# Kernel tuning notes

Measured on AMD Instinct MI355X. Metric: run time of the kernel, lower is better.

Reference implementation:

```python
import jax, jax.numpy as jnp
import numpy as np

NEG_SLOPE = 0.3

def capped_lrelu(x):
    # clamp(LeakyReLU_0.3(x), max=1)
    return jnp.minimum(jnp.where(x >= 0, x, NEG_SLOPE * x), 1.0)

def setup_inputs() -> dict:
    key = jax.random.key(0)
    ks = jax.random.split(key, 8)
    B, T, V, H, O = 64, 512, 512, 256, 512
    s = 1.0 / np.sqrt(H)
    return {
        "sentence": jax.random.normal(ks[0], (B, T, V), dtype=jnp.float32),
        "prev_state": jnp.zeros((1, B, H), dtype=jnp.float32),
        "W_ih": jax.random.normal(ks[1], (H, V), dtype=jnp.float32) * s,
        "b_ih": jax.random.normal(ks[2], (H,), dtype=jnp.float32) * s,
        "W_hh": jax.random.normal(ks[3], (H, H), dtype=jnp.float32) * s,
        "b_hh": jax.random.normal(ks[4], (H,), dtype=jnp.float32) * s,
        "W_out": jax.random.normal(ks[5], (O, H), dtype=jnp.float32) * s,
        "b_out": jax.random.normal(ks[6], (O,), dtype=jnp.float32) * s,
    }

def reference(sentence, prev_state, W_ih, b_ih, W_hh, b_hh, W_out, b_out):
    # nn.RNN(nonlinearity='relu'), batch_first, n_layers=1:
    #   h_t = relu(x_t @ W_ih^T + b_ih + h_{t-1} @ W_hh^T + b_hh)
    # Precompute input projections for all timesteps, scan the recurrence.
    x_proj = jnp.einsum('btv,hv->bth', sentence, W_ih) + b_ih  # [B,T,H]
    x_proj_t = jnp.swapaxes(x_proj, 0, 1)                      # [T,B,H]
    h0 = prev_state[0]                                         # [B,H]

    def step(h, xt):
        h_new = jax.nn.relu(xt + h @ W_hh.T + b_hh)
        return h_new, h_new

    h_last, out_seq = jax.lax.scan(step, h0, x_proj_t)         # [T,B,H]
    out_seq = jnp.swapaxes(out_seq, 0, 1)                      # [B,T,H]

    hidden_activ = capped_lrelu(out_seq)
    tags = jax.nn.sigmoid(jnp.einsum('bth,oh->bto', hidden_activ, W_out) + b_out)
    h_n = h_last[None]                                         # [1,B,H]
    return tags, h_n
```

## Files before the change

### kernel.cpp

```cpp
#include <hip/hip_runtime.h>
#include <hip/hip_bf16.h>


typedef __attribute__((ext_vector_type(8))) _Float16 half8;
typedef __attribute__((ext_vector_type(4))) _Float16 half4;
typedef __attribute__((ext_vector_type(4))) float   floatx4;

__device__ __forceinline__ void lds_barrier() {
    asm volatile("s_waitcnt lgkmcnt(0)\n\ts_barrier" ::: "memory");
}

__global__ void conv_weights(const float* __restrict__ wih, const float* __restrict__ wout,
                             _Float16* __restrict__ out) {
    int idx = blockIdx.x * blockDim.x + threadIdx.x;
    const float* src = (idx < 32768) ? wih : wout;
    int j = idx & 32767;
    float4 v = ((const float4*)src)[j];
    half4 h = { (_Float16)v.x, (_Float16)v.y, (_Float16)v.z, (_Float16)v.w };
    ((half4*)out)[idx] = h;
}

__device__ __forceinline__ void stage_weights_swz(const _Float16* __restrict__ src,
                                                  int rowStrideHalves,
                                                  _Float16* lds) {
    int wave = threadIdx.x >> 6;
    int lane = threadIdx.x & 63;
#pragma unroll
    for (int j = 0; j < 16; j++) {
        int Lb = j * 8192 + wave * 1024 + lane * 16;
        int n  = Lb >> 9;
        int c  = Lb & 511;
        int cs = c ^ ((n & 7) << 4);
        const _Float16* g = src + (size_t)n * rowStrideHalves + (cs >> 1);
        _Float16* l = lds + (j * 8192 + wave * 1024) / 2;
        __builtin_amdgcn_global_load_lds((const __attribute__((address_space(1))) void*)g,
                                         (__attribute__((address_space(3))) void*)l,
                                         16, 0, 0);
    }
    asm volatile("s_waitcnt vmcnt(0)" ::: "memory");
    __syncthreads();
}

__global__ __launch_bounds__(512, 2) void gemm1_xproj(const float* __restrict__ A,
                                                      const _Float16* __restrict__ Bw,
                                                      const float* __restrict__ b_ih,
                                                      const float* __restrict__ b_hh,
                                                      float* __restrict__ C) {
    const int K = 512, N = 256;
    __shared__ _Float16 ldsB[65536];
    int wave = threadIdx.x >> 6;
    int lane = threadIdx.x & 63;
    int row  = lane & 15;
    int quad = lane >> 4;
    int m0 = blockIdx.x * 128 + wave * 16;

    floatx4 acc[16];
#pragma unroll
    for (int i = 0; i < 16; i++) acc[i] = (floatx4){0.f, 0.f, 0.f, 0.f};

    const float* pa = A + (size_t)(m0 + row) * K + quad * 8;
    const char* lb = (const char*)ldsB;

    for (int h = 0; h < 2; h++) {
        if (h) __syncthreads();
        stage_weights_swz(Bw + h * 256, 512, ldsB);

        for (int kk = 0; kk < 256; kk += 32) {
            float4 a0 = *(const float4*)(pa + h * 256 + kk);
            float4 a1 = *(const float4*)(pa + h * 256 + kk + 4);
            half8 a = { (_Float16)a0.x, (_Float16)a0.y, (_Float16)a0.z, (_Float16)a0.w,
                        (_Float16)a1.x, (_Float16)a1.y, (_Float16)a1.z, (_Float16)a1.w };
#pragma unroll
            for (int nt = 0; nt < 16; nt++) {
                int n = nt * 16 + row;
                int byte = n * 512 + ((quad * 16 + kk * 2) ^ ((n & 7) << 4));
                half8 b = *(const half8*)(lb + byte);
                acc[nt] = __builtin_amdgcn_mfma_f32_16x16x32_f16(a, b, acc[nt], 0, 0, 0);
            }
        }
    }
#pragma unroll
    for (int nt = 0; nt < 16; nt++) {
        int n = nt * 16 + row;
        float bn = b_ih[n] + b_hh[n];
#pragma unroll
        for (int r = 0; r < 4; r++) {
            int m = m0 + quad * 4 + r;
            C[(size_t)m * N + n] = acc[nt][r] + bn;
        }
    }
}

__global__ __launch_bounds__(512, 2) void rnn_recur(const float* __restrict__ xp,
                                                    const float* __restrict__ h0,
                                                    const float* __restrict__ W_hh,
                                                    _Float16* __restrict__ hid,
                                                    float* __restrict__ h_n) {
    const int Hh = 256, T = 512, LD = 264;
    int b0   = blockIdx.x * 16;
    int wave = threadIdx.x >> 6;
    int lane = threadIdx.x & 63;
    int c    = lane & 15;
    int q    = lane >> 4;

    half8 wf[2][8];
#pragma unroll
    for (int nt = 0; nt < 2; nt++) {
        int n = (wave * 2 + nt) * 16 + c;
        const float* wr = W_hh + (size_t)n * Hh + q * 8;
#pragma unroll
        for (int kt = 0; kt < 8; kt++) {
            float4 x0 = *(const float4*)(wr + kt * 32);
            float4 x1 = *(const float4*)(wr + kt * 32 + 4);
            wf[nt][kt] = (half8){ (_Float16)x0.x, (_Float16)x0.y, (_Float16)x0.z, (_Float16)x0.w,
                                  (_Float16)x1.x, (_Float16)x1.y, (_Float16)x1.z, (_Float16)x1.w };
        }
    }

    __shared__ _Float16 hb[2][16][264];
    for (int idx = threadIdx.x; idx < 16 * 256; idx += 512) {
        int m = idx >> 8, k = idx & 255;
        hb[0][m][k] = (_Float16)h0[(size_t)(b0 + m) * Hh + k];
    }
    __syncthreads();

    const float* xpb = xp + (size_t)(b0 + c) * T * Hh;
    _Float16* hidb = hid + (size_t)(b0 + c) * T * Hh;

    int noff[2];
#pragma unroll
    for (int nt = 0; nt < 2; nt++) noff[nt] = (wave * 2 + nt) * 16 + q * 4;

    float4 xq0[2], xq1[2];
#pragma unroll
    for (int nt = 0; nt < 2; nt++) {
        xq0[nt] = *(const float4*)(xpb + (size_t)0 * Hh + noff[nt]);
        xq1[nt] = *(const float4*)(xpb + (size_t)1 * Hh + noff[nt]);
    }
    const float* pf0 = xpb + 2 * Hh;
    const float* pf1 = xpb + 3 * Hh;
    _Float16* hp = hidb;

    auto do_step = [&](int parity, float4 (&xq)[2], const float*& pf,
                       bool prefetch, bool last) {
        const _Float16* hr = &hb[parity][0][0];
        floatx4 aA0 = { xq[0].x, xq[0].y, xq[0].z, xq[0].w };
        floatx4 aA1 = { xq[1].x, xq[1].y, xq[1].z, xq[1].w };
        floatx4 aB0 = {0.f,0.f,0.f,0.f}, aB1 = {0.f,0.f,0.f,0.f};
#pragma unroll
        for (int kt = 0; kt < 4; kt++) {
            half8 hfA = *(const half8*)(hr + c * LD + kt * 32 + q * 8);
            half8 hfB = *(const half8*)(hr + c * LD + (kt + 4) * 32 + q * 8);
            aA0 = __builtin_amdgcn_mfma_f32_16x16x32_f16(wf[0][kt],     hfA, aA0, 0, 0, 0);
            aB0 = __builtin_amdgcn_mfma_f32_16x16x32_f16(wf[0][kt + 4], hfB, aB0, 0, 0, 0);
            aA1 = __builtin_amdgcn_mfma_f32_16x16x32_f16(wf[1][kt],     hfA, aA1, 0, 0, 0);
            aB1 = __builtin_amdgcn_mfma_f32_16x16x32_f16(wf[1][kt + 4], hfB, aB1, 0, 0, 0);
        }
        floatx4 acc[2];
        acc[0] = aA0 + aB0;
        acc[1] = aA1 + aB1;

        _Float16* hw = &hb[parity ^ 1][0][0];
#pragma unroll
        for (int nt = 0; nt < 2; nt++) {
            float v0 = fmaxf(acc[nt][0], 0.f);
            float v1 = fmaxf(acc[nt][1], 0.f);
            float v2 = fmaxf(acc[nt][2], 0.f);
            float v3 = fmaxf(acc[nt][3], 0.f);
            half4 hv = { (_Float16)v0, (_Float16)v1, (_Float16)v2, (_Float16)v3 };
            *(half4*)(hw + c * LD + noff[nt]) = hv;
            *(half4*)(hp + noff[nt]) = hv;
            if (last) {
                float4 hn = { v0, v1, v2, v3 };
                *(float4*)(h_n + (size_t)(b0 + c) * Hh + noff[nt]) = hn;
            }
        }
        hp += Hh;
        if (prefetch) {
#pragma unroll
            for (int nt = 0; nt < 2; nt++)
                xq[nt] = *(const float4*)(pf + noff[nt]);
            pf += 2 * Hh;
        }
        lds_barrier();
    };

    for (int t = 0; t < T - 2; t += 2) {
        do_step(0, xq0, pf0, true, false);
        do_step(1, xq1, pf1, true, false);
    }
    do_step(0, xq0, pf0, false, false);
    do_step(1, xq1, pf1, false, true);
}

__global__ __launch_bounds__(512, 2) void gemm3_tags(const _Float16* __restrict__ A,
                                                     const _Float16* __restrict__ Bw,
                                                     const float* __restrict__ bias,
                                                     float* __restrict__ C) {
    const int K = 256, N = 512;
    __shared__ _Float16 ldsB[65536];
    int wave = threadIdx.x >> 6;
    int lane = threadIdx.x & 63;
    int row  = lane & 15;
    int quad = lane >> 4;
    int m0 = blockIdx.x * 128 + wave * 16;
    int nb = blockIdx.y;

    stage_weights_swz(Bw + (size_t)nb * 256 * K, K, ldsB);

    floatx4 acc[16];
#pragma unroll
    for (int i = 0; i < 16; i++) acc[i] = (floatx4){0.f, 0.f, 0.f, 0.f};

    const _Float16* pa = A + (size_t)(m0 + row) * K + quad * 8;
    const char* lb = (const char*)ldsB;
    const _Float16 one = (_Float16)1.0f;

    for (int kk = 0; kk < 256; kk += 32) {
        half8 a = *(const half8*)(pa + kk);
#pragma unroll
        for (int j = 0; j < 8; j++) a[j] = (a[j] < one) ? a[j] : one;
#pragma unroll
        for (int nt = 0; nt < 16; nt++) {
            int n = nt * 16 + row;
            int byte = n * 512 + ((quad * 16 + kk * 2) ^ ((n & 7) << 4));
            half8 b = *(const half8*)(lb + byte);
            acc[nt] = __builtin_amdgcn_mfma_f32_16x16x32_f16(a, b, acc[nt], 0, 0, 0);
        }
    }
#pragma unroll
    for (int nt = 0; nt < 16; nt++) {
        int n = nb * 256 + nt * 16 + row;
        float bn = bias[n];
#pragma unroll
        for (int r = 0; r < 4; r++) {
            int m = m0 + quad * 4 + r;
            float v = acc[nt][r] + bn;
            C[(size_t)m * N + n] = 1.f / (1.f + __expf(-v));
        }
    }
}

extern "C" void kernel_launch(void* const* d_in, const int* in_sizes, int n_in,
                              void* d_out, int out_size, void* d_ws, size_t ws_size,
                              hipStream_t stream) {
    const float* sentence   = (const float*)d_in[0];
    const float* prev_state = (const float*)d_in[1];
    const float* W_ih       = (const float*)d_in[2];
    const float* b_ih       = (const float*)d_in[3];
    const float* W_hh       = (const float*)d_in[4];
    const float* b_hh       = (const float*)d_in[5];
    const float* W_out      = (const float*)d_in[6];
    const float* b_out      = (const float*)d_in[7];

    const size_t WIH_N   = 256u * 512u;
    const size_t WOUT_N  = 512u * 256u;
    const size_t XPROJ_N = 32768u * 256u;
    const size_t HID_N   = 64u * 512u * 256u;

    char* w = (char*)d_ws;
    _Float16* wih_f  = (_Float16*)w;  w += WIH_N * sizeof(_Float16);
    _Float16* wout_f = (_Float16*)w;  w += WOUT_N * sizeof(_Float16);
    float*    xproj  = (float*)w;     w += XPROJ_N * sizeof(float);
    _Float16* hid_f  = (_Float16*)w;  w += HID_N * sizeof(_Float16);

    float* tags = (float*)d_out;
    float* h_n  = (float*)d_out + 16777216;

    conv_weights<<<256, 256, 0, stream>>>(W_ih, W_out, wih_f);

    gemm1_xproj<<<256, 512, 0, stream>>>(sentence, wih_f, b_ih, b_hh, xproj);

    rnn_recur<<<4, 512, 0, stream>>>(xproj, prev_state, W_hh, hid_f, h_n);

    gemm3_tags<<<dim3(256, 2), 512, 0, stream>>>(hid_f, wout_f, b_out, tags);
}
```

Before: 542.6 us.

## Shrink GEMM tiles to 256 threads and move xproj add after recurrence MFMAs

Both GEMMs move from 512-thread blocks with 128KB LDS weight tiles to 256-thread blocks with 64KB tiles. gemm1 now stages K in four 128-wide phases, and gemm3 splits N into four 128-column blocks, so the grids grow to give more blocks and better occupancy on the CUs. In the recurrence, the MFMA accumulators start at zero and the x-projection is added just before the ReLU, which takes the prefetched xproj load off the MFMA dependency chain. The cost is more weight restaging and more barriers per block.

```diff
diff --git a/kernel.cpp b/kernel.cpp
--- a/kernel.cpp
+++ b/kernel.cpp
@@ -20,19 +20,38 @@
     ((half4*)out)[idx] = h;
 }
 
-__device__ __forceinline__ void stage_weights_swz(const _Float16* __restrict__ src,
-                                                  int rowStrideHalves,
-                                                  _Float16* lds) {
+__device__ __forceinline__ void stage_w_256x128(const _Float16* __restrict__ src,
+                                                int rowStrideHalves, _Float16* lds) {
     int wave = threadIdx.x >> 6;
     int lane = threadIdx.x & 63;
 #pragma unroll
     for (int j = 0; j < 16; j++) {
-        int Lb = j * 8192 + wave * 1024 + lane * 16;
+        int Lb = j * 4096 + wave * 1024 + lane * 16;
+        int n  = Lb >> 8;
+        int c  = Lb & 255;
+        int cs = c ^ ((n & 7) << 4);
+        const _Float16* g = src + (size_t)n * rowStrideHalves + (cs >> 1);
+        _Float16* l = lds + (j * 4096 + wave * 1024) / 2;
+        __builtin_amdgcn_global_load_lds((const __attribute__((address_space(1))) void*)g,
+                                         (__attribute__((address_space(3))) void*)l,
+                                         16, 0, 0);
+    }
+    asm volatile("s_waitcnt vmcnt(0)" ::: "memory");
+    __syncthreads();
+}
+
+__device__ __forceinline__ void stage_w_128x256(const _Float16* __restrict__ src,
+                                                int rowStrideHalves, _Float16* lds) {
+    int wave = threadIdx.x >> 6;
+    int lane = threadIdx.x & 63;
+#pragma unroll
+    for (int j = 0; j < 16; j++) {
+        int Lb = j * 4096 + wave * 1024 + lane * 16;
         int n  = Lb >> 9;
         int c  = Lb & 511;
         int cs = c ^ ((n & 7) << 4);
         const _Float16* g = src + (size_t)n * rowStrideHalves + (cs >> 1);
-        _Float16* l = lds + (j * 8192 + wave * 1024) / 2;
+        _Float16* l = lds + (j * 4096 + wave * 1024) / 2;
         __builtin_amdgcn_global_load_lds((const __attribute__((address_space(1))) void*)g,
                                          (__attribute__((address_space(3))) void*)l,
                                          16, 0, 0);
@@ -41,18 +60,18 @@
     __syncthreads();
 }
 
-__global__ __launch_bounds__(512, 2) void gemm1_xproj(const float* __restrict__ A,
+__global__ __launch_bounds__(256, 2) void gemm1_xproj(const float* __restrict__ A,
                                                       const _Float16* __restrict__ Bw,
                                                       const float* __restrict__ b_ih,
                                                       const float* __restrict__ b_hh,
                                                       float* __restrict__ C) {
     const int K = 512, N = 256;
-    __shared__ _Float16 ldsB[65536];
+    __shared__ _Float16 ldsB[32768];
     int wave = threadIdx.x >> 6;
     int lane = threadIdx.x & 63;
     int row  = lane & 15;
     int quad = lane >> 4;
-    int m0 = blockIdx.x * 128 + wave * 16;
+    int m0 = blockIdx.x * 64 + wave * 16;
 
     floatx4 acc[16];
 #pragma unroll
@@ -61,19 +80,19 @@
     const float* pa = A + (size_t)(m0 + row) * K + quad * 8;
     const char* lb = (const char*)ldsB;
 
-    for (int h = 0; h < 2; h++) {
-        if (h) __syncthreads();
-        stage_weights_swz(Bw + h * 256, 512, ldsB);
-
-        for (int kk = 0; kk < 256; kk += 32) {
-            float4 a0 = *(const float4*)(pa + h * 256 + kk);
-            float4 a1 = *(const float4*)(pa + h * 256 + kk + 4);
+    for (int ph = 0; ph < 4; ph++) {
+        if (ph) __syncthreads();
+        stage_w_256x128(Bw + ph * 128, 512, ldsB);
+
+        for (int kk = 0; kk < 128; kk += 32) {
+            float4 a0 = *(const float4*)(pa + ph * 128 + kk);
+            float4 a1 = *(const float4*)(pa + ph * 128 + kk + 4);
             half8 a = { (_Float16)a0.x, (_Float16)a0.y, (_Float16)a0.z, (_Float16)a0.w,
                         (_Float16)a1.x, (_Float16)a1.y, (_Float16)a1.z, (_Float16)a1.w };
 #pragma unroll
             for (int nt = 0; nt < 16; nt++) {
                 int n = nt * 16 + row;
-                int byte = n * 512 + ((quad * 16 + kk * 2) ^ ((n & 7) << 4));
+                int byte = n * 256 + ((quad * 16 + kk * 2) ^ ((n & 7) << 4));
                 half8 b = *(const half8*)(lb + byte);
                 acc[nt] = __builtin_amdgcn_mfma_f32_16x16x32_f16(a, b, acc[nt], 0, 0, 0);
             }
@@ -144,8 +163,7 @@
     auto do_step = [&](int parity, float4 (&xq)[2], const float*& pf,
                        bool prefetch, bool last) {
         const _Float16* hr = &hb[parity][0][0];
-        floatx4 aA0 = { xq[0].x, xq[0].y, xq[0].z, xq[0].w };
-        floatx4 aA1 = { xq[1].x, xq[1].y, xq[1].z, xq[1].w };
+        floatx4 aA0 = {0.f,0.f,0.f,0.f}, aA1 = {0.f,0.f,0.f,0.f};
         floatx4 aB0 = {0.f,0.f,0.f,0.f}, aB1 = {0.f,0.f,0.f,0.f};
 #pragma unroll
         for (int kt = 0; kt < 4; kt++) {
@@ -163,10 +181,10 @@
         _Float16* hw = &hb[parity ^ 1][0][0];
 #pragma unroll
         for (int nt = 0; nt < 2; nt++) {
-            float v0 = fmaxf(acc[nt][0], 0.f);
-            float v1 = fmaxf(acc[nt][1], 0.f);
-            float v2 = fmaxf(acc[nt][2], 0.f);
-            float v3 = fmaxf(acc[nt][3], 0.f);
+            float v0 = fmaxf(acc[nt][0] + xq[nt].x, 0.f);
+            float v1 = fmaxf(acc[nt][1] + xq[nt].y, 0.f);
+            float v2 = fmaxf(acc[nt][2] + xq[nt].z, 0.f);
+            float v3 = fmaxf(acc[nt][3] + xq[nt].w, 0.f);
             half4 hv = { (_Float16)v0, (_Float16)v1, (_Float16)v2, (_Float16)v3 };
             *(half4*)(hw + c * LD + noff[nt]) = hv;
             *(half4*)(hp + noff[nt]) = hv;
@@ -193,24 +211,24 @@
     do_step(1, xq1, pf1, false, true);
 }
 
-__global__ __launch_bounds__(512, 2) void gemm3_tags(const _Float16* __restrict__ A,
+__global__ __launch_bounds__(256, 2) void gemm3_tags(const _Float16* __restrict__ A,
                                                      const _Float16* __restrict__ Bw,
                                                      const float* __restrict__ bias,
                                                      float* __restrict__ C) {
     const int K = 256, N = 512;
-    __shared__ _Float16 ldsB[65536];
+    __shared__ _Float16 ldsB[32768];
     int wave = threadIdx.x >> 6;
     int lane = threadIdx.x & 63;
     int row  = lane & 15;
     int quad = lane >> 4;
-    int m0 = blockIdx.x * 128 + wave * 16;
-    int nb = blockIdx.y;
-
-    stage_weights_swz(Bw + (size_t)nb * 256 * K, K, ldsB);
-
-    floatx4 acc[16];
-#pragma unroll
-    for (int i = 0; i < 16; i++) acc[i] = (floatx4){0.f, 0.f, 0.f, 0.f};
+    int m0 = blockIdx.x * 64 + wave * 16;
+    int nq = blockIdx.y;
+
+    stage_w_128x256(Bw + (size_t)nq * 128 * K, K, ldsB);
+
+    floatx4 acc[8];
+#pragma unroll
+    for (int i = 0; i < 8; i++) acc[i] = (floatx4){0.f, 0.f, 0.f, 0.f};
 
     const _Float16* pa = A + (size_t)(m0 + row) * K + quad * 8;
     const char* lb = (const char*)ldsB;
@@ -221,7 +239,7 @@
 #pragma unroll
         for (int j = 0; j < 8; j++) a[j] = (a[j] < one) ? a[j] : one;
 #pragma unroll
-        for (int nt = 0; nt < 16; nt++) {
+        for (int nt = 0; nt < 8; nt++) {
             int n = nt * 16 + row;
             int byte = n * 512 + ((quad * 16 + kk * 2) ^ ((n & 7) << 4));
             half8 b = *(const half8*)(lb + byte);
@@ -229,8 +247,8 @@
         }
     }
 #pragma unroll
-    for (int nt = 0; nt < 16; nt++) {
-        int n = nb * 256 + nt * 16 + row;
+    for (int nt = 0; nt < 8; nt++) {
+        int n = nq * 128 + nt * 16 + row;
         float bn = bias[n];
 #pragma unroll
         for (int r = 0; r < 4; r++) {
@@ -269,9 +287,9 @@
 
     conv_weights<<<256, 256, 0, stream>>>(W_ih, W_out, wih_f);
 
-    gemm1_xproj<<<256, 512, 0, stream>>>(sentence, wih_f, b_ih, b_hh, xproj);
+    gemm1_xproj<<<512, 256, 0, stream>>>(sentence, wih_f, b_ih, b_hh, xproj);
 
     rnn_recur<<<4, 512, 0, stream>>>(xproj, prev_state, W_hh, hid_f, h_n);
 
-    gemm3_tags<<<dim3(256, 2), 512, 0, stream>>>(hid_f, wout_f, b_out, tags);
-}
+    gemm3_tags<<<dim3(512, 4), 256, 0, stream>>>(hid_f, wout_f, b_out, tags);
+}
```

Result: faster. 524.8 us (-3.3%).

## Halve recurrence block to 4 waves each computing four output tiles

Applied to the files above, without the earlier changes.

The recurrent kernel now runs with 256 threads (4 waves) instead of 512, and each wave holds four 16-column tiles of W_hh in registers instead of two. The per-step barrier then synchronises fewer waves and each wave issues more independent MFMAs per step. The x-projection add is also moved from the accumulator initial value to after the MFMA chain. The cost is twice the register footprint per wave and fewer waves to hide latency on the serial critical path.

```diff
diff --git a/kernel.cpp b/kernel.cpp
--- a/kernel.cpp
+++ b/kernel.cpp
@@ -91,7 +91,7 @@
     }
 }
 
-__global__ __launch_bounds__(512, 2) void rnn_recur(const float* __restrict__ xp,
+__global__ __launch_bounds__(256, 1) void rnn_recur(const float* __restrict__ xp,
                                                     const float* __restrict__ h0,
                                                     const float* __restrict__ W_hh,
                                                     _Float16* __restrict__ hid,
@@ -103,10 +103,10 @@
     int c    = lane & 15;
     int q    = lane >> 4;
 
-    half8 wf[2][8];
-#pragma unroll
-    for (int nt = 0; nt < 2; nt++) {
-        int n = (wave * 2 + nt) * 16 + c;
+    half8 wf[4][8];
+#pragma unroll
+    for (int nt = 0; nt < 4; nt++) {
+        int n = wave * 64 + nt * 16 + c;
         const float* wr = W_hh + (size_t)n * Hh + q * 8;
 #pragma unroll
         for (int kt = 0; kt < 8; kt++) {
@@ -118,7 +118,7 @@
     }
 
     __shared__ _Float16 hb[2][16][264];
-    for (int idx = threadIdx.x; idx < 16 * 256; idx += 512) {
+    for (int idx = threadIdx.x; idx < 16 * 256; idx += 256) {
         int m = idx >> 8, k = idx & 255;
         hb[0][m][k] = (_Float16)h0[(size_t)(b0 + m) * Hh + k];
     }
@@ -127,13 +127,13 @@
     const float* xpb = xp + (size_t)(b0 + c) * T * Hh;
     _Float16* hidb = hid + (size_t)(b0 + c) * T * Hh;
 
-    int noff[2];
-#pragma unroll
-    for (int nt = 0; nt < 2; nt++) noff[nt] = (wave * 2 + nt) * 16 + q * 4;
-
-    float4 xq0[2], xq1[2];
-#pragma unroll
-    for (int nt = 0; nt < 2; nt++) {
+    int noff[4];
+#pragma unroll
+    for (int nt = 0; nt < 4; nt++) noff[nt] = wave * 64 + nt * 16 + q * 4;
+
+    float4 xq0[4], xq1[4];
+#pragma unroll
+    for (int nt = 0; nt < 4; nt++) {
         xq0[nt] = *(const float4*)(xpb + (size_t)0 * Hh + noff[nt]);
         xq1[nt] = *(const float4*)(xpb + (size_t)1 * Hh + noff[nt]);
     }
@@ -141,32 +141,34 @@
     const float* pf1 = xpb + 3 * Hh;
     _Float16* hp = hidb;
 
-    auto do_step = [&](int parity, float4 (&xq)[2], const float*& pf,
+    auto do_step = [&](int parity, float4 (&xq)[4], const float*& pf,
                        bool prefetch, bool last) {
         const _Float16* hr = &hb[parity][0][0];
-        floatx4 aA0 = { xq[0].x, xq[0].y, xq[0].z, xq[0].w };
-        floatx4 aA1 = { xq[1].x, xq[1].y, xq[1].z, xq[1].w };
-        floatx4 aB0 = {0.f,0.f,0.f,0.f}, aB1 = {0.f,0.f,0.f,0.f};
+        floatx4 aA[4], aB[4];
+#pragma unroll
+        for (int nt = 0; nt < 4; nt++) {
+            aA[nt] = (floatx4){0.f,0.f,0.f,0.f};
+            aB[nt] = (floatx4){0.f,0.f,0.f,0.f};
+        }
 #pragma unroll
         for (int kt = 0; kt < 4; kt++) {
             half8 hfA = *(const half8*)(hr + c * LD + kt * 32 + q * 8);
             half8 hfB = *(const half8*)(hr + c * LD + (kt + 4) * 32 + q * 8);
-            aA0 = __builtin_amdgcn_mfma_f32_16x16x32_f16(wf[0][kt],     hfA, aA0, 0, 0, 0);
-            aB0 = __builtin_amdgcn_mfma_f32_16x16x32_f16(wf[0][kt + 4], hfB, aB0, 0, 0, 0);
-            aA1 = __builtin_amdgcn_mfma_f32_16x16x32_f16(wf[1][kt],     hfA, aA1, 0, 0, 0);
-            aB1 = __builtin_amdgcn_mfma_f32_16x16x32_f16(wf[1][kt + 4], hfB, aB1, 0, 0, 0);
-        }
-        floatx4 acc[2];
-        acc[0] = aA0 + aB0;
-        acc[1] = aA1 + aB1;
+#pragma unroll
+            for (int nt = 0; nt < 4; nt++) {
+                aA[nt] = __builtin_amdgcn_mfma_f32_16x16x32_f16(wf[nt][kt],     hfA, aA[nt], 0, 0, 0);
+                aB[nt] = __builtin_amdgcn_mfma_f32_16x16x32_f16(wf[nt][kt + 4], hfB, aB[nt], 0, 0, 0);
+            }
+        }
 
         _Float16* hw = &hb[parity ^ 1][0][0];
 #pragma unroll
-        for (int nt = 0; nt < 2; nt++) {
-            float v0 = fmaxf(acc[nt][0], 0.f);
-            float v1 = fmaxf(acc[nt][1], 0.f);
-            float v2 = fmaxf(acc[nt][2], 0.f);
-            float v3 = fmaxf(acc[nt][3], 0.f);
+        for (int nt = 0; nt < 4; nt++) {
+            floatx4 acc = aA[nt] + aB[nt];
+            float v0 = fmaxf(acc[0] + xq[nt].x, 0.f);
+            float v1 = fmaxf(acc[1] + xq[nt].y, 0.f);
+            float v2 = fmaxf(acc[2] + xq[nt].z, 0.f);
+            float v3 = fmaxf(acc[3] + xq[nt].w, 0.f);
             half4 hv = { (_Float16)v0, (_Float16)v1, (_Float16)v2, (_Float16)v3 };
             *(half4*)(hw + c * LD + noff[nt]) = hv;
             *(half4*)(hp + noff[nt]) = hv;
@@ -178,7 +180,7 @@
         hp += Hh;
         if (prefetch) {
 #pragma unroll
-            for (int nt = 0; nt < 2; nt++)
+            for (int nt = 0; nt < 4; nt++)
                 xq[nt] = *(const float4*)(pf + noff[nt]);
             pf += 2 * Hh;
         }
@@ -271,7 +273,7 @@
 
     gemm1_xproj<<<256, 512, 0, stream>>>(sentence, wih_f, b_ih, b_hh, xproj);
 
-    rnn_recur<<<4, 512, 0, stream>>>(xproj, prev_state, W_hh, hid_f, h_n);
+    rnn_recur<<<4, 256, 0, stream>>>(xproj, prev_state, W_hh, hid_f, h_n);
 
     gemm3_tags<<<dim3(256, 2), 512, 0, stream>>>(hid_f, wout_f, b_out, tags);
 }
```

After: 619.1 us. 1.14x slower.
